# Kernel tuning notes

Hardware: AMD Instinct MI355X
Metric: run time of the kernel (lower is better)

The kernel has to match this reference:

```python
import jax, jax.numpy as jnp
import numpy as np

B, L, E, H = 2, 2048, 1024, 16
D = E // H


def setup_inputs() -> dict:
    key = jax.random.key(0)
    ks = jax.random.split(key, 6)
    s = 1.0 / np.sqrt(E)
    return {
        "X": jax.random.normal(ks[0], (B, L, E), dtype=jnp.float32),
        "ke_bias": jax.random.normal(ks[1], (B * H, L, L), dtype=jnp.float32) * 0.05,
        "in_proj_w": jax.random.normal(ks[2], (3 * E, E), dtype=jnp.float32) * s,
        "in_proj_b": jnp.zeros((3 * E,), dtype=jnp.float32),
        "out_proj_w": jax.random.normal(ks[3], (E, E), dtype=jnp.float32) * s,
        "out_proj_b": jnp.zeros((E,), dtype=jnp.float32),
    }


def reference(X, ke_bias, in_proj_w, in_proj_b, out_proj_w, out_proj_b):
    # Packed QKV projection, matching nn.MultiheadAttention layout.
    qkv = X @ in_proj_w.T + in_proj_b  # [B, L, 3E]
    q, k, v = jnp.split(qkv, 3, axis=-1)
    # [B, L, E] -> [B, H, L, D]
    q = q.reshape(B, L, H, D).transpose(0, 2, 1, 3)
    k = k.reshape(B, L, H, D).transpose(0, 2, 1, 3)
    v = v.reshape(B, L, H, D).transpose(0, 2, 1, 3)
    scale = 1.0 / jnp.sqrt(jnp.asarray(D, dtype=q.dtype))
    scores = jnp.einsum("bhqd,bhkd->bhqk", q * scale, k)
    scores = scores + ke_bias.reshape(B, H, L, L)  # additive knowledge bias
    A = jax.nn.softmax(scores, axis=-1)
    ctx = jnp.einsum("bhqk,bhkd->bhqd", A, v)  # [B, H, L, D]
    ctx = ctx.transpose(0, 2, 1, 3).reshape(B, L, E)
    return ctx @ out_proj_w.T + out_proj_b
```

## Files before the change

kernel.cpp:

```cpp
#include <hip/hip_runtime.h>
#include <stdint.h>

typedef __attribute__((ext_vector_type(4))) float f32x4;
typedef __attribute__((ext_vector_type(8))) short bf16x8;

#define MFMA(a, b, c) __builtin_amdgcn_mfma_f32_16x16x32_bf16(a, b, c, 0, 0, 0)

__device__ __forceinline__ short f2bf(float f) {
    unsigned u = __builtin_bit_cast(unsigned, f);
    u = (u + 0x7fffu + ((u >> 16) & 1u)) >> 16;
    return (short)u;
}

__device__ __forceinline__ void g2l16(const void* g, void* l) {
    __builtin_amdgcn_global_load_lds(
        (const __attribute__((address_space(1))) unsigned*)g,
        (__attribute__((address_space(3))) unsigned*)l, 16, 0, 0);
}

__global__ void cvt_bf16_kernel(const float* __restrict__ src,
                                short* __restrict__ dst, int n8) {
    int i = blockIdx.x * blockDim.x + threadIdx.x;
    if (i >= n8) return;
    const f32x4* s = (const f32x4*)src;
    f32x4 a = s[2 * i], b = s[2 * i + 1];
    bf16x8 o;
    o[0] = f2bf(a[0]); o[1] = f2bf(a[1]); o[2] = f2bf(a[2]); o[3] = f2bf(a[3]);
    o[4] = f2bf(b[0]); o[5] = f2bf(b[1]); o[6] = f2bf(b[2]); o[7] = f2bf(b[3]);
    ((bf16x8*)dst)[i] = o;
}

__global__ __launch_bounds__(256, 2) void gemm_qkv_kernel(
    const short* __restrict__ A, const short* __restrict__ W,
    const float* __restrict__ bias,
    short* __restrict__ qb, short* __restrict__ kb, short* __restrict__ vtb) {
    __shared__ short As[128 * 32];
    __shared__ short Bs[128 * 32];
    const int tid = threadIdx.x;
    const int wave = tid >> 6, lane = tid & 63;
    const int al = lane >> 4, ac = lane & 15;
    const int m0 = blockIdx.x * 128;
    const int n0 = blockIdx.y * 128;
    const int wm = wave & 1, wn = wave >> 1;

    const int crow = tid >> 2, ccol = (tid & 3) * 8;
    const short* Ag0 = A + (m0 + crow) * 1024 + ccol;
    const short* Ag1 = A + (m0 + crow + 64) * 1024 + ccol;
    const short* Wg0 = W + (n0 + crow) * 1024 + ccol;
    const short* Wg1 = W + (n0 + crow + 64) * 1024 + ccol;
    short* lA0 = &As[wave * 512];
    short* lA1 = &As[2048 + wave * 512];
    short* lB0 = &Bs[wave * 512];
    short* lB1 = &Bs[2048 + wave * 512];

    f32x4 acc[4][4];
#pragma unroll
    for (int mi = 0; mi < 4; mi++)
#pragma unroll
        for (int ni = 0; ni < 4; ni++) acc[mi][ni] = (f32x4){0.f, 0.f, 0.f, 0.f};

    for (int k0 = 0; k0 < 1024; k0 += 32) {
        __syncthreads();
        g2l16(Ag0 + k0, lA0);
        g2l16(Ag1 + k0, lA1);
        g2l16(Wg0 + k0, lB0);
        g2l16(Wg1 + k0, lB1);
        __syncthreads();
        bf16x8 af[4], bf[4];
#pragma unroll
        for (int i = 0; i < 4; i++) {
            af[i] = *(const bf16x8*)&As[(wm * 64 + i * 16 + ac) * 32 + al * 8];
            bf[i] = *(const bf16x8*)&Bs[(wn * 64 + i * 16 + ac) * 32 + al * 8];
        }
#pragma unroll
        for (int mi = 0; mi < 4; mi++)
#pragma unroll
            for (int ni = 0; ni < 4; ni++)
                acc[mi][ni] = MFMA(af[mi], bf[ni], acc[mi][ni]);
    }

    const int which = (n0 + wn * 64) >> 10;
#pragma unroll
    for (int mi = 0; mi < 4; mi++) {
#pragma unroll
        for (int ni = 0; ni < 4; ni++) {
            const int col = n0 + wn * 64 + ni * 16 + ac;
            const int e = col & 1023;
            const int h = e >> 6, d = e & 63;
            const float bv = bias[col];
#pragma unroll
            for (int r = 0; r < 4; r++) {
                const int row = m0 + wm * 64 + mi * 16 + al * 4 + r;
                const int b = row >> 11, l = row & 2047;
                const int bh = b * 16 + h;
                const float v = acc[mi][ni][r] + bv;
                if (which == 0)
                    qb[(bh * 2048 + l) * 64 + d] = f2bf(v * 0.125f);
                else if (which == 1)
                    kb[(bh * 2048 + l) * 64 + d] = f2bf(v);
                else
                    vtb[(bh * 64 + d) * 2048 + l] = f2bf(v);
            }
        }
    }
}

__global__ __launch_bounds__(256, 4) void attn_kernel(
    const short* __restrict__ Qb, const short* __restrict__ Kb,
    const short* __restrict__ Vtb, const float* __restrict__ bias,
    short* __restrict__ Ctx) {
    __shared__ short Qs[64 * 72];
    __shared__ short Ks[64 * 72];
    __shared__ short Vs[64 * 72];
    __shared__ short Ps[4][16 * 72];
    const int tid = threadIdx.x;
    const int wave = tid >> 6, lane = tid & 63;
    const int al = lane >> 4, ac = lane & 15;
    const int q0 = blockIdx.x * 64;
    const int bh = blockIdx.y;
    const long long kvbase = (long long)bh * (2048 * 64);

    const int sr = tid >> 3, sg = (tid & 7) * 8;

    *(bf16x8*)&Qs[sr * 72 + sg] = *(const bf16x8*)&Qb[kvbase + (q0 + sr) * 64 + sg];
    *(bf16x8*)&Qs[(sr + 32) * 72 + sg] =
        *(const bf16x8*)&Qb[kvbase + (q0 + sr + 32) * 64 + sg];
    __syncthreads();
    const bf16x8 qf0 = *(const bf16x8*)&Qs[(wave * 16 + ac) * 72 + al * 8];
    const bf16x8 qf1 = *(const bf16x8*)&Qs[(wave * 16 + ac) * 72 + al * 8 + 32];

    float m_i[4], l_i[4];
    f32x4 o[4];
#pragma unroll
    for (int r = 0; r < 4; r++) { m_i[r] = -1e30f; l_i[r] = 0.f; }
#pragma unroll
    for (int ni = 0; ni < 4; ni++) o[ni] = (f32x4){0.f, 0.f, 0.f, 0.f};

    const float L2E = 1.44269504088896340736f;
    const float* biasrow =
        bias + ((long long)bh * 2048 + q0 + wave * 16 + al * 4) * 2048;

    for (int kb = 0; kb < 32; ++kb) {
        const int k0 = kb * 64;
        __syncthreads();
        *(bf16x8*)&Ks[sr * 72 + sg] =
            *(const bf16x8*)&Kb[kvbase + (k0 + sr) * 64 + sg];
        *(bf16x8*)&Ks[(sr + 32) * 72 + sg] =
            *(const bf16x8*)&Kb[kvbase + (k0 + sr + 32) * 64 + sg];
        *(bf16x8*)&Vs[sr * 72 + sg] =
            *(const bf16x8*)&Vtb[kvbase + sr * 2048 + k0 + sg];
        *(bf16x8*)&Vs[(sr + 32) * 72 + sg] =
            *(const bf16x8*)&Vtb[kvbase + (sr + 32) * 2048 + k0 + sg];
        __syncthreads();

        f32x4 s[4];
#pragma unroll
        for (int ni = 0; ni < 4; ni++) {
            const bf16x8 kf0 = *(const bf16x8*)&Ks[(ni * 16 + ac) * 72 + al * 8];
            const bf16x8 kf1 =
                *(const bf16x8*)&Ks[(ni * 16 + ac) * 72 + al * 8 + 32];
            s[ni] = MFMA(qf0, kf0, ((f32x4){0.f, 0.f, 0.f, 0.f}));
            s[ni] = MFMA(qf1, kf1, s[ni]);
        }
        float mloc[4] = {-1e30f, -1e30f, -1e30f, -1e30f};
#pragma unroll
        for (int ni = 0; ni < 4; ni++)
#pragma unroll
            for (int r = 0; r < 4; r++) {
                float v = (s[ni][r] + biasrow[r * 2048 + k0 + ni * 16 + ac]) * L2E;
                s[ni][r] = v;
                mloc[r] = fmaxf(mloc[r], v);
            }
#pragma unroll
        for (int r = 0; r < 4; r++) {
#pragma unroll
            for (int off = 1; off < 16; off <<= 1)
                mloc[r] = fmaxf(mloc[r], __shfl_xor(mloc[r], off));
            const float mn = fmaxf(m_i[r], mloc[r]);
            const float a = __builtin_exp2f(m_i[r] - mn);
            m_i[r] = mn;
            l_i[r] *= a;
#pragma unroll
            for (int ni = 0; ni < 4; ni++) o[ni][r] *= a;
        }
        float rs[4] = {0.f, 0.f, 0.f, 0.f};
#pragma unroll
        for (int ni = 0; ni < 4; ni++)
#pragma unroll
            for (int r = 0; r < 4; r++) {
                const float p = __builtin_exp2f(s[ni][r] - m_i[r]);
                rs[r] += p;
                Ps[wave][(al * 4 + r) * 72 + ni * 16 + ac] = f2bf(p);
            }
#pragma unroll
        for (int r = 0; r < 4; r++) {
#pragma unroll
            for (int off = 1; off < 16; off <<= 1) rs[r] += __shfl_xor(rs[r], off);
            l_i[r] += rs[r];
        }
        const bf16x8 pf0 = *(const bf16x8*)&Ps[wave][ac * 72 + al * 8];
        const bf16x8 pf1 = *(const bf16x8*)&Ps[wave][ac * 72 + al * 8 + 32];
#pragma unroll
        for (int ni = 0; ni < 4; ni++) {
            const bf16x8 vf0 = *(const bf16x8*)&Vs[(ni * 16 + ac) * 72 + al * 8];
            const bf16x8 vf1 =
                *(const bf16x8*)&Vs[(ni * 16 + ac) * 72 + al * 8 + 32];
            o[ni] = MFMA(pf0, vf0, o[ni]);
            o[ni] = MFMA(pf1, vf1, o[ni]);
        }
    }

    const int b = bh >> 4, h = bh & 15;
#pragma unroll
    for (int r = 0; r < 4; r++) {
        const float inv = 1.f / l_i[r];
        const int qrow = q0 + wave * 16 + al * 4 + r;
#pragma unroll
        for (int ni = 0; ni < 4; ni++) {
            const int d = ni * 16 + ac;
            Ctx[((long long)(b * 2048 + qrow)) * 1024 + h * 64 + d] =
                f2bf(o[ni][r] * inv);
        }
    }
}

__global__ __launch_bounds__(256, 2) void gemm_out_kernel(
    const short* __restrict__ A, const short* __restrict__ W,
    const float* __restrict__ bias, float* __restrict__ out) {
    __shared__ short As[128 * 32];
    __shared__ short Bs[128 * 32];
    const int tid = threadIdx.x;
    const int wave = tid >> 6, lane = tid & 63;
    const int al = lane >> 4, ac = lane & 15;
    const int m0 = blockIdx.x * 128;
    const int n0 = blockIdx.y * 128;
    const int wm = wave & 1, wn = wave >> 1;

    const int crow = tid >> 2, ccol = (tid & 3) * 8;
    const short* Ag0 = A + (m0 + crow) * 1024 + ccol;
    const short* Ag1 = A + (m0 + crow + 64) * 1024 + ccol;
    const short* Wg0 = W + (n0 + crow) * 1024 + ccol;
    const short* Wg1 = W + (n0 + crow + 64) * 1024 + ccol;
    short* lA0 = &As[wave * 512];
    short* lA1 = &As[2048 + wave * 512];
    short* lB0 = &Bs[wave * 512];
    short* lB1 = &Bs[2048 + wave * 512];

    f32x4 acc[4][4];
#pragma unroll
    for (int mi = 0; mi < 4; mi++)
#pragma unroll
        for (int ni = 0; ni < 4; ni++) acc[mi][ni] = (f32x4){0.f, 0.f, 0.f, 0.f};

    for (int k0 = 0; k0 < 1024; k0 += 32) {
        __syncthreads();
        g2l16(Ag0 + k0, lA0);
        g2l16(Ag1 + k0, lA1);
        g2l16(Wg0 + k0, lB0);
        g2l16(Wg1 + k0, lB1);
        __syncthreads();
        bf16x8 af[4], bf[4];
#pragma unroll
        for (int i = 0; i < 4; i++) {
            af[i] = *(const bf16x8*)&As[(wm * 64 + i * 16 + ac) * 32 + al * 8];
            bf[i] = *(const bf16x8*)&Bs[(wn * 64 + i * 16 + ac) * 32 + al * 8];
        }
#pragma unroll
        for (int mi = 0; mi < 4; mi++)
#pragma unroll
            for (int ni = 0; ni < 4; ni++)
                acc[mi][ni] = MFMA(af[mi], bf[ni], acc[mi][ni]);
    }

#pragma unroll
    for (int mi = 0; mi < 4; mi++) {
#pragma unroll
        for (int ni = 0; ni < 4; ni++) {
            const int col = n0 + wn * 64 + ni * 16 + ac;
            const float bv = bias[col];
#pragma unroll
            for (int r = 0; r < 4; r++) {
                const int row = m0 + wm * 64 + mi * 16 + al * 4 + r;
                out[row * 1024 + col] = acc[mi][ni][r] + bv;
            }
        }
    }
}

extern "C" void kernel_launch(void* const* d_in, const int* in_sizes, int n_in,
                              void* d_out, int out_size, void* d_ws,
                              size_t ws_size, hipStream_t stream) {
    const float* X = (const float*)d_in[0];
    const float* keb = (const float*)d_in[1];
    const float* Wi = (const float*)d_in[2];
    const float* bi = (const float*)d_in[3];
    const float* Wo = (const float*)d_in[4];
    const float* bo = (const float*)d_in[5];
    float* out = (float*)d_out;

    char* ws = (char*)d_ws;
    short* Xb  = (short*)(ws);
    short* Wib = (short*)(ws + 8388608);
    short* Wob = (short*)(ws + 14680064);
    short* Qb  = (short*)(ws + 16777216);
    short* Kb  = (short*)(ws + 25165824);
    short* Vtb = (short*)(ws + 33554432);
    short* Ctx = (short*)(ws + 41943040);

    cvt_bf16_kernel<<<dim3(524288 / 256), 256, 0, stream>>>(X, Xb, 524288);
    cvt_bf16_kernel<<<dim3(393216 / 256), 256, 0, stream>>>(Wi, Wib, 393216);
    cvt_bf16_kernel<<<dim3(131072 / 256), 256, 0, stream>>>(Wo, Wob, 131072);
    gemm_qkv_kernel<<<dim3(32, 24), 256, 0, stream>>>(Xb, Wib, bi, Qb, Kb, Vtb);
    attn_kernel<<<dim3(32, 32), 256, 0, stream>>>(Qb, Kb, Vtb, keb, Ctx);
    gemm_out_kernel<<<dim3(32, 8), 256, 0, stream>>>(Ctx, Wob, bo, out);
}
```

Before: 966.9 us.

## Vectorize GEMM epilogue stores via LDS and prefetch K/V/bias in attention

The QKV and output GEMM epilogues now stage each 16x16 accumulator tile through a per-wave LDS scratch buffer. This lets every lane write contiguous 4-element vectors instead of scattered scalar stores, including the transposed V layout. The attention kernel adds register-level software prefetch of the next K/V tile and the next bias block, so global loads overlap with the current tile's compute. The prefetch raises register pressure at 4 waves per SIMD, and the scratch round trips rely on wave-local ordering without explicit barriers.

```diff
diff --git a/kernel.cpp b/kernel.cpp
--- a/kernel.cpp
+++ b/kernel.cpp
@@ -3,6 +3,7 @@
 
 typedef __attribute__((ext_vector_type(4))) float f32x4;
 typedef __attribute__((ext_vector_type(8))) short bf16x8;
+typedef __attribute__((ext_vector_type(4))) short bf16x4;
 
 #define MFMA(a, b, c) __builtin_amdgcn_mfma_f32_16x16x32_bf16(a, b, c, 0, 0, 0)
 
@@ -36,6 +37,7 @@
     short* __restrict__ qb, short* __restrict__ kb, short* __restrict__ vtb) {
     __shared__ short As[128 * 32];
     __shared__ short Bs[128 * 32];
+    __shared__ short scrS[4][16 * 24];
     const int tid = threadIdx.x;
     const int wave = tid >> 6, lane = tid & 63;
     const int al = lane >> 4, ac = lane & 15;
@@ -66,40 +68,57 @@
         g2l16(Wg0 + k0, lB0);
         g2l16(Wg1 + k0, lB1);
         __syncthreads();
-        bf16x8 af[4], bf[4];
+        bf16x8 af[4], bfr[4];
 #pragma unroll
         for (int i = 0; i < 4; i++) {
             af[i] = *(const bf16x8*)&As[(wm * 64 + i * 16 + ac) * 32 + al * 8];
-            bf[i] = *(const bf16x8*)&Bs[(wn * 64 + i * 16 + ac) * 32 + al * 8];
+            bfr[i] = *(const bf16x8*)&Bs[(wn * 64 + i * 16 + ac) * 32 + al * 8];
         }
 #pragma unroll
         for (int mi = 0; mi < 4; mi++)
 #pragma unroll
             for (int ni = 0; ni < 4; ni++)
-                acc[mi][ni] = MFMA(af[mi], bf[ni], acc[mi][ni]);
-    }
-
-    const int which = (n0 + wn * 64) >> 10;
+                acc[mi][ni] = MFMA(af[mi], bfr[ni], acc[mi][ni]);
+    }
+
+    const int n0w = n0 + wn * 64;
+    const int which = n0w >> 10;
+    short* scr = scrS[wave];
+    const int lr = lane >> 2;
+    const int lq = lane & 3;
+    const int bglob = m0 >> 11;
+
 #pragma unroll
     for (int mi = 0; mi < 4; mi++) {
 #pragma unroll
         for (int ni = 0; ni < 4; ni++) {
-            const int col = n0 + wn * 64 + ni * 16 + ac;
-            const int e = col & 1023;
-            const int h = e >> 6, d = e & 63;
-            const float bv = bias[col];
-#pragma unroll
-            for (int r = 0; r < 4; r++) {
-                const int row = m0 + wm * 64 + mi * 16 + al * 4 + r;
-                const int b = row >> 11, l = row & 2047;
-                const int bh = b * 16 + h;
-                const float v = acc[mi][ni][r] + bv;
-                if (which == 0)
-                    qb[(bh * 2048 + l) * 64 + d] = f2bf(v * 0.125f);
-                else if (which == 1)
-                    kb[(bh * 2048 + l) * 64 + d] = f2bf(v);
-                else
-                    vtb[(bh * 64 + d) * 2048 + l] = f2bf(v);
+            const int col0 = n0w + ni * 16;
+            const float bvc = bias[col0 + ac];
+            if (which == 2) {
+                bf16x4 pk;
+#pragma unroll
+                for (int r = 0; r < 4; r++) pk[r] = f2bf(acc[mi][ni][r] + bvc);
+                *(bf16x4*)&scr[ac * 24 + al * 4] = pk;
+                bf16x4 v4 = *(const bf16x4*)&scr[lr * 24 + lq * 4];
+                const int colv = col0 + lr;
+                const int e = colv & 1023;
+                const int h = e >> 6, d = e & 63;
+                const int row0 = m0 + wm * 64 + mi * 16 + lq * 4;
+                const int l0 = row0 & 2047;
+                *(bf16x4*)&vtb[(((bglob * 16 + h) * 64 + d) * 2048) + l0] = v4;
+            } else {
+                const float sc = (which == 0) ? 0.125f : 1.0f;
+#pragma unroll
+                for (int r = 0; r < 4; r++)
+                    scr[(al * 4 + r) * 24 + ac] = f2bf((acc[mi][ni][r] + bvc) * sc);
+                bf16x4 v4 = *(const bf16x4*)&scr[lr * 24 + lq * 4];
+                const int col = col0 + lq * 4;
+                const int e = col & 1023;
+                const int h = e >> 6, d0 = e & 63;
+                const int row = m0 + wm * 64 + mi * 16 + lr;
+                const int l = row & 2047;
+                short* dst = (which == 0) ? qb : kb;
+                *(bf16x4*)&dst[(((bglob * 16 + h) * 2048 + l) * 64) + d0] = v4;
             }
         }
     }
@@ -137,21 +156,35 @@
     for (int ni = 0; ni < 4; ni++) o[ni] = (f32x4){0.f, 0.f, 0.f, 0.f};
 
     const float L2E = 1.44269504088896340736f;
-    const float* biasrow =
-        bias + ((long long)bh * 2048 + q0 + wave * 16 + al * 4) * 2048;
-
-    for (int kb = 0; kb < 32; ++kb) {
-        const int k0 = kb * 64;
-        __syncthreads();
-        *(bf16x8*)&Ks[sr * 72 + sg] =
-            *(const bf16x8*)&Kb[kvbase + (k0 + sr) * 64 + sg];
-        *(bf16x8*)&Ks[(sr + 32) * 72 + sg] =
-            *(const bf16x8*)&Kb[kvbase + (k0 + sr + 32) * 64 + sg];
-        *(bf16x8*)&Vs[sr * 72 + sg] =
-            *(const bf16x8*)&Vtb[kvbase + sr * 2048 + k0 + sg];
-        *(bf16x8*)&Vs[(sr + 32) * 72 + sg] =
-            *(const bf16x8*)&Vtb[kvbase + (sr + 32) * 2048 + k0 + sg];
-        __syncthreads();
+    const float* bp =
+        bias + ((long long)bh * 2048 + q0 + wave * 16 + al * 4) * 2048 + ac;
+
+    bf16x8 kr0 = *(const bf16x8*)&Kb[kvbase + sr * 64 + sg];
+    bf16x8 kr1 = *(const bf16x8*)&Kb[kvbase + (sr + 32) * 64 + sg];
+    bf16x8 vr0 = *(const bf16x8*)&Vtb[kvbase + sr * 2048 + sg];
+    bf16x8 vr1 = *(const bf16x8*)&Vtb[kvbase + (sr + 32) * 2048 + sg];
+    float bc[16];
+#pragma unroll
+    for (int ni = 0; ni < 4; ni++)
+#pragma unroll
+        for (int r = 0; r < 4; r++) bc[ni * 4 + r] = bp[r * 2048 + ni * 16];
+
+#pragma unroll 2
+    for (int kbk = 0; kbk < 32; ++kbk) {
+        __syncthreads();
+        *(bf16x8*)&Ks[sr * 72 + sg] = kr0;
+        *(bf16x8*)&Ks[(sr + 32) * 72 + sg] = kr1;
+        *(bf16x8*)&Vs[sr * 72 + sg] = vr0;
+        *(bf16x8*)&Vs[(sr + 32) * 72 + sg] = vr1;
+        __syncthreads();
+
+        const int k1 = (kbk + 1) * 64;
+        if (kbk < 31) {
+            kr0 = *(const bf16x8*)&Kb[kvbase + (k1 + sr) * 64 + sg];
+            kr1 = *(const bf16x8*)&Kb[kvbase + (k1 + sr + 32) * 64 + sg];
+            vr0 = *(const bf16x8*)&Vtb[kvbase + sr * 2048 + k1 + sg];
+            vr1 = *(const bf16x8*)&Vtb[kvbase + (sr + 32) * 2048 + k1 + sg];
+        }
 
         f32x4 s[4];
 #pragma unroll
@@ -167,7 +200,7 @@
         for (int ni = 0; ni < 4; ni++)
 #pragma unroll
             for (int r = 0; r < 4; r++) {
-                float v = (s[ni][r] + biasrow[r * 2048 + k0 + ni * 16 + ac]) * L2E;
+                float v = (s[ni][r] + bc[ni * 4 + r]) * L2E;
                 s[ni][r] = v;
                 mloc[r] = fmaxf(mloc[r], v);
             }
@@ -198,6 +231,16 @@
             for (int off = 1; off < 16; off <<= 1) rs[r] += __shfl_xor(rs[r], off);
             l_i[r] += rs[r];
         }
+
+        float bn[16];
+        if (kbk < 31) {
+#pragma unroll
+            for (int ni = 0; ni < 4; ni++)
+#pragma unroll
+                for (int r = 0; r < 4; r++)
+                    bn[ni * 4 + r] = bp[r * 2048 + k1 + ni * 16];
+        }
+
         const bf16x8 pf0 = *(const bf16x8*)&Ps[wave][ac * 72 + al * 8];
         const bf16x8 pf1 = *(const bf16x8*)&Ps[wave][ac * 72 + al * 8 + 32];
 #pragma unroll
@@ -208,6 +251,8 @@
             o[ni] = MFMA(pf0, vf0, o[ni]);
             o[ni] = MFMA(pf1, vf1, o[ni]);
         }
+#pragma unroll
+        for (int i = 0; i < 16; i++) bc[i] = bn[i];
     }
 
     const int b = bh >> 4, h = bh & 15;
@@ -229,6 +274,7 @@
     const float* __restrict__ bias, float* __restrict__ out) {
     __shared__ short As[128 * 32];
     __shared__ short Bs[128 * 32];
+    __shared__ float scrF[4][16 * 28];
     const int tid = threadIdx.x;
     const int wave = tid >> 6, lane = tid & 63;
     const int al = lane >> 4, ac = lane & 15;
@@ -259,30 +305,33 @@
         g2l16(Wg0 + k0, lB0);
         g2l16(Wg1 + k0, lB1);
         __syncthreads();
-        bf16x8 af[4], bf[4];
+        bf16x8 af[4], bfr[4];
 #pragma unroll
         for (int i = 0; i < 4; i++) {
             af[i] = *(const bf16x8*)&As[(wm * 64 + i * 16 + ac) * 32 + al * 8];
-            bf[i] = *(const bf16x8*)&Bs[(wn * 64 + i * 16 + ac) * 32 + al * 8];
+            bfr[i] = *(const bf16x8*)&Bs[(wn * 64 + i * 16 + ac) * 32 + al * 8];
         }
 #pragma unroll
         for (int mi = 0; mi < 4; mi++)
 #pragma unroll
             for (int ni = 0; ni < 4; ni++)
-                acc[mi][ni] = MFMA(af[mi], bf[ni], acc[mi][ni]);
-    }
-
+                acc[mi][ni] = MFMA(af[mi], bfr[ni], acc[mi][ni]);
+    }
+
+    float* scr = scrF[wave];
+    const int lr = lane >> 2, lq = lane & 3;
 #pragma unroll
     for (int mi = 0; mi < 4; mi++) {
 #pragma unroll
         for (int ni = 0; ni < 4; ni++) {
-            const int col = n0 + wn * 64 + ni * 16 + ac;
-            const float bv = bias[col];
-#pragma unroll
-            for (int r = 0; r < 4; r++) {
-                const int row = m0 + wm * 64 + mi * 16 + al * 4 + r;
-                out[row * 1024 + col] = acc[mi][ni][r] + bv;
-            }
+            const int col0 = n0 + wn * 64 + ni * 16;
+            const float bvc = bias[col0 + ac];
+#pragma unroll
+            for (int r = 0; r < 4; r++)
+                scr[(al * 4 + r) * 28 + ac] = acc[mi][ni][r] + bvc;
+            f32x4 v4 = *(const f32x4*)&scr[lr * 28 + lq * 4];
+            const int row = m0 + wm * 64 + mi * 16 + lr;
+            *(f32x4*)&out[row * 1024 + col0 + lq * 4] = v4;
         }
     }
 }
```

Result: faster. 805.4 us (-16.7%).
